# Kernel optimization log

Hardware: AMD Instinct MI355X
Metric: run time of the kernel (lower is better)

The kernel has to match this reference:

```python
import jax, jax.numpy as jnp
import numpy as np

B, C, D, O = 262144, 256, 64, 8


def setup_inputs() -> dict:
    key = jax.random.key(0)
    k1, k2, k3, k4 = jax.random.split(key, 4)
    inputs = jax.random.normal(k1, (B, D), dtype=jnp.float32)
    cluster_centers = jax.random.normal(k2, (C, D), dtype=jnp.float32)
    # widths initialized ~ N(1.0, 0.05) as in the layer
    widths = 1.0 + 0.05 * jax.random.normal(k3, (C,), dtype=jnp.float32)
    # rule_weights ~ N(0, 0.05)
    rule_weights = 0.05 * jax.random.normal(k4, (C, O), dtype=jnp.float32)
    return {"inputs": inputs, "cluster_centers": cluster_centers,
            "widths": widths, "rule_weights": rule_weights}


def reference(inputs, cluster_centers, widths, rule_weights):
    # Squared L2 distances via ||a-c||^2 = ||a||^2 + ||c||^2 - 2 a.c
    # (avoids materializing the [B, C, D] broadcast diff tensor)
    x_sq = jnp.sum(inputs * inputs, axis=1, keepdims=True)          # [B, 1]
    c_sq = jnp.sum(cluster_centers * cluster_centers, axis=1)       # [C]
    cross = inputs @ cluster_centers.T                               # [B, C]
    dists_squared = x_sq + c_sq[None, :] - 2.0 * cross               # [B, C]
    # Gaussian membership with per-cluster widths
    memb = jnp.exp(-dists_squared / (2.0 * widths * widths))         # [B, C]
    # Normalize over clusters (sum-normalization, not softmax-of-logits)
    memb_norm = memb / jnp.sum(memb, axis=1, keepdims=True)          # [B, C]
    # Weighted rule consequents
    return memb_norm @ rule_weights                                  # [B, O]
```

## Files before the change

### kernel.cpp

```cpp
#include <hip/hip_runtime.h>


#define NB 262144
#define NC 256
#define ND 64
#define NO 8

typedef __attribute__((ext_vector_type(8))) short short8;
typedef __attribute__((ext_vector_type(8))) _Float16 half8;
typedef __attribute__((ext_vector_type(16))) float floatx16;

#define WOFF 20480
#define WS_SHORTS 28672

__device__ inline unsigned short f2bf(float f) {
    unsigned u = __builtin_bit_cast(unsigned, f);
    u = u + 0x7FFFu + ((u >> 16) & 1u);
    return (unsigned short)(u >> 16);
}

__global__ __launch_bounds__(512, 4) void fuzzy_main(
    const float* __restrict__ x,
    const float* __restrict__ centers,
    const float* __restrict__ widths,
    const float* __restrict__ W,
    float* __restrict__ out) {
    __shared__ short lds_s[WS_SHORTS];

    const int tid = threadIdx.x;
    const int wave = tid >> 6;
    const int lane = tid & 63;
    const int col = lane & 31;
    const int h = lane >> 5;
    const int bbase = (blockIdx.x * 8 + wave) * 64;

    float4 xr[2][8];
#pragma unroll
    for (int u = 0; u < 2; ++u) {
        const float4* xp = (const float4*)(x + (size_t)(bbase + u * 32 + col) * ND);
#pragma unroll
        for (int kd = 0; kd < 4; ++kd) {
            xr[u][2 * kd + 0] = xp[4 * kd + 2 * h + 0];
            xr[u][2 * kd + 1] = xp[4 * kd + 2 * h + 1];
        }
    }

    {
        const int t = wave;
        const int c = 32 * t + ((col & 19) | ((col & 4) << 1) | ((col & 8) >> 1));
        const float* cr = centers + c * ND;
        float vv[4][8];
        float part = 0.0f;
#pragma unroll
        for (int kd = 0; kd < 4; ++kd) {
            const float4* p = (const float4*)(cr + kd * 16 + h * 8);
            float4 a0 = p[0], a1 = p[1];
            vv[kd][0] = a0.x; vv[kd][1] = a0.y; vv[kd][2] = a0.z; vv[kd][3] = a0.w;
            vv[kd][4] = a1.x; vv[kd][5] = a1.y; vv[kd][6] = a1.z; vv[kd][7] = a1.w;
#pragma unroll
            for (int j = 0; j < 8; ++j) part = fmaf(vv[kd][j], vv[kd][j], part);
        }
        float csq = part + __shfl_xor(part, 32, 64);
        float w = widths[c];
        float kk = 1.4426950408889634f / (2.0f * w * w);

#pragma unroll
        for (int kd = 0; kd < 4; ++kd) {
            half8 ah;
#pragma unroll
            for (int j = 0; j < 8; ++j) ah[j] = (_Float16)(2.0f * kk * vv[kd][j]);
            *(half8*)&lds_s[((t * 5 + kd) * 64 + lane) * 8] = ah;
        }
        half8 av;
#pragma unroll
        for (int j = 0; j < 8; ++j) av[j] = (_Float16)0.0f;
        if (h == 0) {
            float kh = (float)(_Float16)kk;
            float kl = kk - kh;
            float Bc = csq * kk;
            float Bh = (float)(_Float16)Bc;
            float Bl = Bc - Bh;
            av[0] = (_Float16)(-kh);
            av[1] = (_Float16)(-kh);
            av[2] = (_Float16)(-kl);
            av[3] = (_Float16)(-Bh);
            av[4] = (_Float16)(-Bl);
        }
        *(half8*)&lds_s[((t * 5 + 4) * 64 + lane) * 8] = av;

#pragma unroll
        for (int q = 0; q < 2; ++q) {
            int k2 = 2 * t + q;
            short8 wf;
#pragma unroll
            for (int j = 0; j < 8; ++j) {
                int c2 = k2 * 16 + h * 8 + j;
                float val = (col < NO) ? W[c2 * NO + col] : (col == 8 ? 1.0f : 0.0f);
                wf[j] = (short)f2bf(val);
            }
            *(short8*)&lds_s[WOFF + (k2 * 64 + lane) * 8] = wf;
        }
    }

    half8 xh[2][4];
    half8 f12[2];
#pragma unroll
    for (int u = 0; u < 2; ++u) {
        float part = 0.0f;
#pragma unroll
        for (int kd = 0; kd < 4; ++kd) {
            float4 v0 = xr[u][2 * kd], v1 = xr[u][2 * kd + 1];
            float v[8] = {v0.x, v0.y, v0.z, v0.w, v1.x, v1.y, v1.z, v1.w};
            half8 hh;
#pragma unroll
            for (int j = 0; j < 8; ++j) {
                part = fmaf(v[j], v[j], part);
                hh[j] = (_Float16)v[j];
            }
            xh[u][kd] = hh;
        }
        float xsq = part + __shfl_xor(part, 32, 64);
        float sh = (float)(_Float16)xsq;
        float sl = xsq - sh;
        half8 f;
#pragma unroll
        for (int j = 0; j < 8; ++j) f[j] = (_Float16)0.0f;
        if (h == 0) {
            f[0] = (_Float16)sh;
            f[1] = (_Float16)sl;
            f[2] = (_Float16)sh;
            f[3] = (_Float16)1.0f;
            f[4] = (_Float16)1.0f;
        }
        f12[u] = f;
    }

    __syncthreads();

    floatx16 acc2[2];
#pragma unroll
    for (int u = 0; u < 2; ++u)
#pragma unroll
        for (int i = 0; i < 16; ++i) acc2[u][i] = 0.0f;

#pragma unroll 2
    for (int t = 0; t < 8; ++t) {
        const half8 A0 = *(const half8*)&lds_s[((t * 5 + 0) * 64 + lane) * 8];
        const half8 A1 = *(const half8*)&lds_s[((t * 5 + 1) * 64 + lane) * 8];
        const half8 A2 = *(const half8*)&lds_s[((t * 5 + 2) * 64 + lane) * 8];
        const half8 A3 = *(const half8*)&lds_s[((t * 5 + 3) * 64 + lane) * 8];
        const half8 C12 = *(const half8*)&lds_s[((t * 5 + 4) * 64 + lane) * 8];
        const short8 w0 = *(const short8*)&lds_s[WOFF + ((2 * t + 0) * 64 + lane) * 8];
        const short8 w1 = *(const short8*)&lds_s[WOFF + ((2 * t + 1) * 64 + lane) * 8];

#pragma unroll
        for (int u = 0; u < 2; ++u) {
            floatx16 acc;
#pragma unroll
            for (int i = 0; i < 16; ++i) acc[i] = 0.0f;
            acc = __builtin_amdgcn_mfma_f32_32x32x16_f16(A0, xh[u][0], acc, 0, 0, 0);
            acc = __builtin_amdgcn_mfma_f32_32x32x16_f16(A1, xh[u][1], acc, 0, 0, 0);
            acc = __builtin_amdgcn_mfma_f32_32x32x16_f16(A2, xh[u][2], acc, 0, 0, 0);
            acc = __builtin_amdgcn_mfma_f32_32x32x16_f16(A3, xh[u][3], acc, 0, 0, 0);
            acc = __builtin_amdgcn_mfma_f32_32x32x16_f16(C12, f12[u], acc, 0, 0, 0);

            unsigned p0 = __builtin_bit_cast(unsigned, __builtin_amdgcn_exp2f(acc[0]));
            unsigned p1 = __builtin_bit_cast(unsigned, __builtin_amdgcn_exp2f(acc[1]));
            unsigned p2 = __builtin_bit_cast(unsigned, __builtin_amdgcn_exp2f(acc[2]));
            unsigned p3 = __builtin_bit_cast(unsigned, __builtin_amdgcn_exp2f(acc[3]));
            unsigned p4 = __builtin_bit_cast(unsigned, __builtin_amdgcn_exp2f(acc[4]));
            unsigned p5 = __builtin_bit_cast(unsigned, __builtin_amdgcn_exp2f(acc[5]));
            unsigned p6 = __builtin_bit_cast(unsigned, __builtin_amdgcn_exp2f(acc[6]));
            unsigned p7 = __builtin_bit_cast(unsigned, __builtin_amdgcn_exp2f(acc[7]));
            unsigned p8 = __builtin_bit_cast(unsigned, __builtin_amdgcn_exp2f(acc[8]));
            unsigned p9 = __builtin_bit_cast(unsigned, __builtin_amdgcn_exp2f(acc[9]));
            unsigned pa = __builtin_bit_cast(unsigned, __builtin_amdgcn_exp2f(acc[10]));
            unsigned pb = __builtin_bit_cast(unsigned, __builtin_amdgcn_exp2f(acc[11]));
            unsigned pc = __builtin_bit_cast(unsigned, __builtin_amdgcn_exp2f(acc[12]));
            unsigned pd = __builtin_bit_cast(unsigned, __builtin_amdgcn_exp2f(acc[13]));
            unsigned pe = __builtin_bit_cast(unsigned, __builtin_amdgcn_exp2f(acc[14]));
            unsigned pf = __builtin_bit_cast(unsigned, __builtin_amdgcn_exp2f(acc[15]));
            uint4 q0, q1;
            q0.x = __builtin_amdgcn_perm(p1, p0, 0x07060302u);
            q0.y = __builtin_amdgcn_perm(p3, p2, 0x07060302u);
            q0.z = __builtin_amdgcn_perm(p5, p4, 0x07060302u);
            q0.w = __builtin_amdgcn_perm(p7, p6, 0x07060302u);
            q1.x = __builtin_amdgcn_perm(p9, p8, 0x07060302u);
            q1.y = __builtin_amdgcn_perm(pb, pa, 0x07060302u);
            q1.z = __builtin_amdgcn_perm(pd, pc, 0x07060302u);
            q1.w = __builtin_amdgcn_perm(pf, pe, 0x07060302u);
            short8 pf0 = __builtin_bit_cast(short8, q0);
            short8 pf1 = __builtin_bit_cast(short8, q1);

            acc2[u] = __builtin_amdgcn_mfma_f32_32x32x16_bf16(w0, pf0, acc2[u], 0, 0, 0);
            acc2[u] = __builtin_amdgcn_mfma_f32_32x32x16_bf16(w1, pf1, acc2[u], 0, 0, 0);
        }
    }

#pragma unroll
    for (int u = 0; u < 2; ++u) {
        float S = acc2[u][4];
        float Sp = __shfl_xor(S, 32, 64);
        if (h) S = Sp;
        float inv = 1.0f / S;
        float4 r;
        r.x = acc2[u][0] * inv;
        r.y = acc2[u][1] * inv;
        r.z = acc2[u][2] * inv;
        r.w = acc2[u][3] * inv;
        ((float4*)(out + (size_t)(bbase + u * 32 + col) * NO))[h] = r;
    }
}

extern "C" void kernel_launch(void* const* d_in, const int* in_sizes, int n_in,
                              void* d_out, int out_size, void* d_ws, size_t ws_size,
                              hipStream_t stream) {
    const float* x       = (const float*)d_in[0];
    const float* centers = (const float*)d_in[1];
    const float* widths  = (const float*)d_in[2];
    const float* W       = (const float*)d_in[3];
    float* out = (float*)d_out;
    (void)d_ws; (void)ws_size;

    fuzzy_main<<<NB / 512, 512, 0, stream>>>(x, centers, widths, W, out);
}
```

Baseline: 113.4 us.

## Process four row tiles per wave with software-pipelined x prefetch

Each wave now handles 128 rows (four 32-row tiles) instead of 64, and the grid is halved, so the per-block setup of the LDS center/weight fragments is amortized over twice as many rows. The x loads for later tiles are issued ahead of the compute of earlier tiles to overlap global memory latency with MFMA and exp work. Launch bounds drop from 4 to 2 blocks per CU to allow more registers for the prefetched tiles. This lowers occupancy and halves the block count, which may reduce latency hiding and load balance across CUs.

```diff
diff --git a/kernel.cpp b/kernel.cpp
--- a/kernel.cpp
+++ b/kernel.cpp
@@ -19,7 +19,124 @@
     return (unsigned short)(u >> 16);
 }
 
-__global__ __launch_bounds__(512, 4) void fuzzy_main(
+struct Raw8 { float4 r0, r1, r2, r3, r4, r5, r6, r7; };
+struct XF { half8 k0, k1, k2, k3, f12; };
+
+__device__ __forceinline__ Raw8 load_x(const float* __restrict__ xrow, int h) {
+    const float4* xp = (const float4*)xrow;
+    Raw8 r;
+    r.r0 = xp[0 + 2 * h]; r.r1 = xp[1 + 2 * h];
+    r.r2 = xp[4 + 2 * h]; r.r3 = xp[5 + 2 * h];
+    r.r4 = xp[8 + 2 * h]; r.r5 = xp[9 + 2 * h];
+    r.r6 = xp[12 + 2 * h]; r.r7 = xp[13 + 2 * h];
+    return r;
+}
+
+__device__ __forceinline__ half8 cvt8(float4 a, float4 b, float& part) {
+    float v[8] = {a.x, a.y, a.z, a.w, b.x, b.y, b.z, b.w};
+    half8 hh;
+#pragma unroll
+    for (int j = 0; j < 8; ++j) {
+        part = fmaf(v[j], v[j], part);
+        hh[j] = (_Float16)v[j];
+    }
+    return hh;
+}
+
+__device__ __forceinline__ XF convert_x(const Raw8& r, int h) {
+    float part = 0.0f;
+    XF f;
+    f.k0 = cvt8(r.r0, r.r1, part);
+    f.k1 = cvt8(r.r2, r.r3, part);
+    f.k2 = cvt8(r.r4, r.r5, part);
+    f.k3 = cvt8(r.r6, r.r7, part);
+    float xsq = part + __shfl_xor(part, 32, 64);
+    float sh = (float)(_Float16)xsq;
+    float sl = xsq - sh;
+    half8 ff;
+#pragma unroll
+    for (int j = 0; j < 8; ++j) ff[j] = (_Float16)0.0f;
+    if (h == 0) {
+        ff[0] = (_Float16)sh;
+        ff[1] = (_Float16)sl;
+        ff[2] = (_Float16)sh;
+        ff[3] = (_Float16)1.0f;
+        ff[4] = (_Float16)1.0f;
+    }
+    f.f12 = ff;
+    return f;
+}
+
+__device__ __forceinline__ void compute_btile(const short* lds_s, int lane, int h,
+                                              const XF& xf, float* __restrict__ outp) {
+    floatx16 acc2;
+#pragma unroll
+    for (int i = 0; i < 16; ++i) acc2[i] = 0.0f;
+
+#pragma unroll
+    for (int t = 0; t < 8; ++t) {
+        const half8 A0 = *(const half8*)&lds_s[((t * 5 + 0) * 64 + lane) * 8];
+        const half8 A1 = *(const half8*)&lds_s[((t * 5 + 1) * 64 + lane) * 8];
+        const half8 A2 = *(const half8*)&lds_s[((t * 5 + 2) * 64 + lane) * 8];
+        const half8 A3 = *(const half8*)&lds_s[((t * 5 + 3) * 64 + lane) * 8];
+        const half8 C12 = *(const half8*)&lds_s[((t * 5 + 4) * 64 + lane) * 8];
+        const short8 w0 = *(const short8*)&lds_s[WOFF + ((2 * t + 0) * 64 + lane) * 8];
+        const short8 w1 = *(const short8*)&lds_s[WOFF + ((2 * t + 1) * 64 + lane) * 8];
+
+        floatx16 acc;
+#pragma unroll
+        for (int i = 0; i < 16; ++i) acc[i] = 0.0f;
+        acc = __builtin_amdgcn_mfma_f32_32x32x16_f16(A0, xf.k0, acc, 0, 0, 0);
+        acc = __builtin_amdgcn_mfma_f32_32x32x16_f16(A1, xf.k1, acc, 0, 0, 0);
+        acc = __builtin_amdgcn_mfma_f32_32x32x16_f16(A2, xf.k2, acc, 0, 0, 0);
+        acc = __builtin_amdgcn_mfma_f32_32x32x16_f16(A3, xf.k3, acc, 0, 0, 0);
+        acc = __builtin_amdgcn_mfma_f32_32x32x16_f16(C12, xf.f12, acc, 0, 0, 0);
+
+        unsigned p0 = __builtin_bit_cast(unsigned, __builtin_amdgcn_exp2f(acc[0]));
+        unsigned p1 = __builtin_bit_cast(unsigned, __builtin_amdgcn_exp2f(acc[1]));
+        unsigned p2 = __builtin_bit_cast(unsigned, __builtin_amdgcn_exp2f(acc[2]));
+        unsigned p3 = __builtin_bit_cast(unsigned, __builtin_amdgcn_exp2f(acc[3]));
+        unsigned p4 = __builtin_bit_cast(unsigned, __builtin_amdgcn_exp2f(acc[4]));
+        unsigned p5 = __builtin_bit_cast(unsigned, __builtin_amdgcn_exp2f(acc[5]));
+        unsigned p6 = __builtin_bit_cast(unsigned, __builtin_amdgcn_exp2f(acc[6]));
+        unsigned p7 = __builtin_bit_cast(unsigned, __builtin_amdgcn_exp2f(acc[7]));
+        unsigned p8 = __builtin_bit_cast(unsigned, __builtin_amdgcn_exp2f(acc[8]));
+        unsigned p9 = __builtin_bit_cast(unsigned, __builtin_amdgcn_exp2f(acc[9]));
+        unsigned pa = __builtin_bit_cast(unsigned, __builtin_amdgcn_exp2f(acc[10]));
+        unsigned pb = __builtin_bit_cast(unsigned, __builtin_amdgcn_exp2f(acc[11]));
+        unsigned pc = __builtin_bit_cast(unsigned, __builtin_amdgcn_exp2f(acc[12]));
+        unsigned pd = __builtin_bit_cast(unsigned, __builtin_amdgcn_exp2f(acc[13]));
+        unsigned pe = __builtin_bit_cast(unsigned, __builtin_amdgcn_exp2f(acc[14]));
+        unsigned pf = __builtin_bit_cast(unsigned, __builtin_amdgcn_exp2f(acc[15]));
+        uint4 q0, q1;
+        q0.x = __builtin_amdgcn_perm(p1, p0, 0x07060302u);
+        q0.y = __builtin_amdgcn_perm(p3, p2, 0x07060302u);
+        q0.z = __builtin_amdgcn_perm(p5, p4, 0x07060302u);
+        q0.w = __builtin_amdgcn_perm(p7, p6, 0x07060302u);
+        q1.x = __builtin_amdgcn_perm(p9, p8, 0x07060302u);
+        q1.y = __builtin_amdgcn_perm(pb, pa, 0x07060302u);
+        q1.z = __builtin_amdgcn_perm(pd, pc, 0x07060302u);
+        q1.w = __builtin_amdgcn_perm(pf, pe, 0x07060302u);
+        short8 pf0 = __builtin_bit_cast(short8, q0);
+        short8 pf1 = __builtin_bit_cast(short8, q1);
+
+        acc2 = __builtin_amdgcn_mfma_f32_32x32x16_bf16(w0, pf0, acc2, 0, 0, 0);
+        acc2 = __builtin_amdgcn_mfma_f32_32x32x16_bf16(w1, pf1, acc2, 0, 0, 0);
+    }
+
+    float S = acc2[4];
+    float Sp = __shfl_xor(S, 32, 64);
+    if (h) S = Sp;
+    float inv = 1.0f / S;
+    float4 r;
+    r.x = acc2[0] * inv;
+    r.y = acc2[1] * inv;
+    r.z = acc2[2] * inv;
+    r.w = acc2[3] * inv;
+    ((float4*)outp)[h] = r;
+}
+
+__global__ __launch_bounds__(512, 2) void fuzzy_main(
     const float* __restrict__ x,
     const float* __restrict__ centers,
     const float* __restrict__ widths,
@@ -32,18 +149,19 @@
     const int lane = tid & 63;
     const int col = lane & 31;
     const int h = lane >> 5;
-    const int bbase = (blockIdx.x * 8 + wave) * 64;
-
-    float4 xr[2][8];
-#pragma unroll
-    for (int u = 0; u < 2; ++u) {
-        const float4* xp = (const float4*)(x + (size_t)(bbase + u * 32 + col) * ND);
-#pragma unroll
-        for (int kd = 0; kd < 4; ++kd) {
-            xr[u][2 * kd + 0] = xp[4 * kd + 2 * h + 0];
-            xr[u][2 * kd + 1] = xp[4 * kd + 2 * h + 1];
-        }
-    }
+    const int bbase = (blockIdx.x * 8 + wave) * 128;
+
+    const float* xr0p = x + (size_t)(bbase + 0 * 32 + col) * ND;
+    const float* xr1p = x + (size_t)(bbase + 1 * 32 + col) * ND;
+    const float* xr2p = x + (size_t)(bbase + 2 * 32 + col) * ND;
+    const float* xr3p = x + (size_t)(bbase + 3 * 32 + col) * ND;
+    float* o0 = out + (size_t)(bbase + 0 * 32 + col) * NO;
+    float* o1 = out + (size_t)(bbase + 1 * 32 + col) * NO;
+    float* o2 = out + (size_t)(bbase + 2 * 32 + col) * NO;
+    float* o3 = out + (size_t)(bbase + 3 * 32 + col) * NO;
+
+    Raw8 ra = load_x(xr0p, h);
+    Raw8 rb = load_x(xr1p, h);
 
     {
         const int t = wave;
@@ -102,114 +220,21 @@
         }
     }
 
-    half8 xh[2][4];
-    half8 f12[2];
-#pragma unroll
-    for (int u = 0; u < 2; ++u) {
-        float part = 0.0f;
-#pragma unroll
-        for (int kd = 0; kd < 4; ++kd) {
-            float4 v0 = xr[u][2 * kd], v1 = xr[u][2 * kd + 1];
-            float v[8] = {v0.x, v0.y, v0.z, v0.w, v1.x, v1.y, v1.z, v1.w};
-            half8 hh;
-#pragma unroll
-            for (int j = 0; j < 8; ++j) {
-                part = fmaf(v[j], v[j], part);
-                hh[j] = (_Float16)v[j];
-            }
-            xh[u][kd] = hh;
-        }
-        float xsq = part + __shfl_xor(part, 32, 64);
-        float sh = (float)(_Float16)xsq;
-        float sl = xsq - sh;
-        half8 f;
-#pragma unroll
-        for (int j = 0; j < 8; ++j) f[j] = (_Float16)0.0f;
-        if (h == 0) {
-            f[0] = (_Float16)sh;
-            f[1] = (_Float16)sl;
-            f[2] = (_Float16)sh;
-            f[3] = (_Float16)1.0f;
-            f[4] = (_Float16)1.0f;
-        }
-        f12[u] = f;
-    }
-
+    XF x0 = convert_x(ra, h);
     __syncthreads();
 
-    floatx16 acc2[2];
-#pragma unroll
-    for (int u = 0; u < 2; ++u)
-#pragma unroll
-        for (int i = 0; i < 16; ++i) acc2[u][i] = 0.0f;
-
-#pragma unroll 2
-    for (int t = 0; t < 8; ++t) {
-        const half8 A0 = *(const half8*)&lds_s[((t * 5 + 0) * 64 + lane) * 8];
-        const half8 A1 = *(const half8*)&lds_s[((t * 5 + 1) * 64 + lane) * 8];
-        const half8 A2 = *(const half8*)&lds_s[((t * 5 + 2) * 64 + lane) * 8];
-        const half8 A3 = *(const half8*)&lds_s[((t * 5 + 3) * 64 + lane) * 8];
-        const half8 C12 = *(const half8*)&lds_s[((t * 5 + 4) * 64 + lane) * 8];
-        const short8 w0 = *(const short8*)&lds_s[WOFF + ((2 * t + 0) * 64 + lane) * 8];
-        const short8 w1 = *(const short8*)&lds_s[WOFF + ((2 * t + 1) * 64 + lane) * 8];
-
-#pragma unroll
-        for (int u = 0; u < 2; ++u) {
-            floatx16 acc;
-#pragma unroll
-            for (int i = 0; i < 16; ++i) acc[i] = 0.0f;
-            acc = __builtin_amdgcn_mfma_f32_32x32x16_f16(A0, xh[u][0], acc, 0, 0, 0);
-            acc = __builtin_amdgcn_mfma_f32_32x32x16_f16(A1, xh[u][1], acc, 0, 0, 0);
-            acc = __builtin_amdgcn_mfma_f32_32x32x16_f16(A2, xh[u][2], acc, 0, 0, 0);
-            acc = __builtin_amdgcn_mfma_f32_32x32x16_f16(A3, xh[u][3], acc, 0, 0, 0);
-            acc = __builtin_amdgcn_mfma_f32_32x32x16_f16(C12, f12[u], acc, 0, 0, 0);
-
-            unsigned p0 = __builtin_bit_cast(unsigned, __builtin_amdgcn_exp2f(acc[0]));
-            unsigned p1 = __builtin_bit_cast(unsigned, __builtin_amdgcn_exp2f(acc[1]));
-            unsigned p2 = __builtin_bit_cast(unsigned, __builtin_amdgcn_exp2f(acc[2]));
-            unsigned p3 = __builtin_bit_cast(unsigned, __builtin_amdgcn_exp2f(acc[3]));
-            unsigned p4 = __builtin_bit_cast(unsigned, __builtin_amdgcn_exp2f(acc[4]));
-            unsigned p5 = __builtin_bit_cast(unsigned, __builtin_amdgcn_exp2f(acc[5]));
-            unsigned p6 = __builtin_bit_cast(unsigned, __builtin_amdgcn_exp2f(acc[6]));
-            unsigned p7 = __builtin_bit_cast(unsigned, __builtin_amdgcn_exp2f(acc[7]));
-            unsigned p8 = __builtin_bit_cast(unsigned, __builtin_amdgcn_exp2f(acc[8]));
-            unsigned p9 = __builtin_bit_cast(unsigned, __builtin_amdgcn_exp2f(acc[9]));
-            unsigned pa = __builtin_bit_cast(unsigned, __builtin_amdgcn_exp2f(acc[10]));
-            unsigned pb = __builtin_bit_cast(unsigned, __builtin_amdgcn_exp2f(acc[11]));
-            unsigned pc = __builtin_bit_cast(unsigned, __builtin_amdgcn_exp2f(acc[12]));
-            unsigned pd = __builtin_bit_cast(unsigned, __builtin_amdgcn_exp2f(acc[13]));
-            unsigned pe = __builtin_bit_cast(unsigned, __builtin_amdgcn_exp2f(acc[14]));
-            unsigned pf = __builtin_bit_cast(unsigned, __builtin_amdgcn_exp2f(acc[15]));
-            uint4 q0, q1;
-            q0.x = __builtin_amdgcn_perm(p1, p0, 0x07060302u);
-            q0.y = __builtin_amdgcn_perm(p3, p2, 0x07060302u);
-            q0.z = __builtin_amdgcn_perm(p5, p4, 0x07060302u);
-            q0.w = __builtin_amdgcn_perm(p7, p6, 0x07060302u);
-            q1.x = __builtin_amdgcn_perm(p9, p8, 0x07060302u);
-            q1.y = __builtin_amdgcn_perm(pb, pa, 0x07060302u);
-            q1.z = __builtin_amdgcn_perm(pd, pc, 0x07060302u);
-            q1.w = __builtin_amdgcn_perm(pf, pe, 0x07060302u);
-            short8 pf0 = __builtin_bit_cast(short8, q0);
-            short8 pf1 = __builtin_bit_cast(short8, q1);
-
-            acc2[u] = __builtin_amdgcn_mfma_f32_32x32x16_bf16(w0, pf0, acc2[u], 0, 0, 0);
-            acc2[u] = __builtin_amdgcn_mfma_f32_32x32x16_bf16(w1, pf1, acc2[u], 0, 0, 0);
-        }
-    }
-
-#pragma unroll
-    for (int u = 0; u < 2; ++u) {
-        float S = acc2[u][4];
-        float Sp = __shfl_xor(S, 32, 64);
-        if (h) S = Sp;
-        float inv = 1.0f / S;
-        float4 r;
-        r.x = acc2[u][0] * inv;
-        r.y = acc2[u][1] * inv;
-        r.z = acc2[u][2] * inv;
-        r.w = acc2[u][3] * inv;
-        ((float4*)(out + (size_t)(bbase + u * 32 + col) * NO))[h] = r;
-    }
+    Raw8 rc = load_x(xr2p, h);
+    compute_btile(lds_s, lane, h, x0, o0);
+
+    XF x1 = convert_x(rb, h);
+    Raw8 rd = load_x(xr3p, h);
+    compute_btile(lds_s, lane, h, x1, o1);
+
+    XF x2 = convert_x(rc, h);
+    compute_btile(lds_s, lane, h, x2, o2);
+
+    XF x3 = convert_x(rd, h);
+    compute_btile(lds_s, lane, h, x3, o3);
 }
 
 extern "C" void kernel_launch(void* const* d_in, const int* in_sizes, int n_in,
@@ -222,5 +247,5 @@
     float* out = (float*)d_out;
     (void)d_ws; (void)ws_size;
 
-    fuzzy_main<<<NB / 512, 512, 0, stream>>>(x, centers, widths, W, out);
-}
+    fuzzy_main<<<NB / 1024, 512, 0, stream>>>(x, centers, widths, W, out);
+}
```

Result: slower. 149.1 us (+31.4%).
